# Kernel optimization log

Measured on AMD Instinct MI355X. Metric: run time of the kernel, lower is better.

Reference implementation:

```python
import jax, jax.numpy as jnp
import numpy as np

NUM_GRAPHS = 1024

def setup_inputs() -> dict:
    key = jax.random.key(0)
    ks = jax.random.split(key, 6)
    N, E = 500000, 16000000
    x = jax.random.normal(ks[0], (N, 4), dtype=jnp.float32)
    edge_index = jax.random.randint(ks[1], (2, E), 0, N, dtype=jnp.int32)
    batch = jnp.sort(jax.random.randint(ks[2], (N,), 0, NUM_GRAPHS, dtype=jnp.int32))
    eps = jnp.zeros((), dtype=jnp.float32)
    W1 = jax.random.normal(ks[3], (4, 16), dtype=jnp.float32) * 0.5
    b1 = jnp.zeros((16,), dtype=jnp.float32)
    W2 = jax.random.normal(ks[4], (16, 4), dtype=jnp.float32) * 0.25
    b2 = jnp.zeros((4,), dtype=jnp.float32)
    return {"x": x, "edge_index": edge_index, "batch": batch,
            "eps": eps, "W1": W1, "b1": b1, "W2": W2, "b2": b2}

def reference(x, edge_index, batch, eps, W1, b1, W2, b2):
    N = x.shape[0]
    src, dst = edge_index[0], edge_index[1]
    # GINConv aggregation: sum of neighbor (source) features at each target node
    agg = jax.ops.segment_sum(x[src], dst, num_segments=N)  # [N, 4]
    h = (1.0 + eps) * x + agg
    # 2-layer MLP: Lin(4,16) -> ReLU -> Lin(16,4)
    h = jax.nn.relu(h @ W1 + b1) @ W2 + b2
    h = jax.nn.relu(h)
    # global_mean_pool over batch segment ids
    sums = jax.ops.segment_sum(h, batch, num_segments=NUM_GRAPHS)      # [G, 4]
    cnts = jax.ops.segment_sum(jnp.ones((N,), h.dtype), batch, num_segments=NUM_GRAPHS)
    pooled = sums / jnp.maximum(cnts, 1.0)[:, None]
    return jax.nn.log_softmax(pooled, axis=1)
```

## Files before the change

kernel.cpp:

```cpp
#include <hip/hip_runtime.h>

#define NUM_GRAPHS 1024
#define BIN_BITS 10
#define BIN_SIZE (1 << BIN_BITS)
#define EB 8192
#define STH 512
#define EPT 16
#define ATH 1024
#define ACH 8192
#define AEPT (ACH / ATH)

typedef int v4i __attribute__((ext_vector_type(4)));

__device__ inline unsigned bf16_rn(float f) {
    unsigned u = __float_as_uint(f);
    return (u + 0x7FFFu + ((u >> 16) & 1u)) >> 16;
}
__global__ void prep_kernel(const float4* __restrict__ x, uint2* __restrict__ x16,
                            int N, int* __restrict__ cursor,
                            float* __restrict__ gsum, float* __restrict__ gcnt,
                            int cap) {
    int i = blockIdx.x * blockDim.x + threadIdx.x;
    if (i < 512) cursor[i] = i * cap;
    if (i < NUM_GRAPHS * 4) gsum[i] = 0.0f;
    if (i < NUM_GRAPHS) gcnt[i] = 0.0f;
    if (i < N) {
        float4 v = x[i];
        uint2 r;
        r.x = bf16_rn(v.x) | (bf16_rn(v.y) << 16);
        r.y = bf16_rn(v.z) | (bf16_rn(v.w) << 16);
        x16[i] = r;
    }
}

__global__ void __launch_bounds__(STH) bin_scatter(const int* __restrict__ src,
                                                   const int* __restrict__ dst,
                                                   int* __restrict__ packed,
                                                   int* __restrict__ cursor,
                                                   int E, int cap, int nb) {
    __shared__ int shist[512];
    __shared__ int sprefix[513];
    __shared__ int sgbase[512];
    __shared__ int spacked[EB];
    __shared__ unsigned short sbin[EB];
    __shared__ int wsum[8];

    const int t = threadIdx.x;
    const int lane = t & 63;
    const int wave = t >> 6;
    const int b0 = blockIdx.x * EB;
    const int myBase = b0 + t * EPT;

    for (int j = t; j < 512; j += STH) shist[j] = 0;
    __syncthreads();

    int pv[EPT];
    int bl[EPT];
    const bool full = (myBase + EPT <= E);
    if (full) {
#pragma unroll
        for (int v = 0; v < EPT / 4; ++v) {
            int4 d = *(const int4*)(dst + myBase + v * 4);
            int4 s = *(const int4*)(src + myBase + v * 4);
            int bn, lp;
            bn = ((unsigned)d.x) >> BIN_BITS; lp = atomicAdd(&shist[bn], 1);
            pv[v * 4 + 0] = ((d.x & (BIN_SIZE - 1)) << 19) | s.x;
            bl[v * 4 + 0] = (bn << 13) | lp;
            bn = ((unsigned)d.y) >> BIN_BITS; lp = atomicAdd(&shist[bn], 1);
            pv[v * 4 + 1] = ((d.y & (BIN_SIZE - 1)) << 19) | s.y;
            bl[v * 4 + 1] = (bn << 13) | lp;
            bn = ((unsigned)d.z) >> BIN_BITS; lp = atomicAdd(&shist[bn], 1);
            pv[v * 4 + 2] = ((d.z & (BIN_SIZE - 1)) << 19) | s.z;
            bl[v * 4 + 2] = (bn << 13) | lp;
            bn = ((unsigned)d.w) >> BIN_BITS; lp = atomicAdd(&shist[bn], 1);
            pv[v * 4 + 3] = ((d.w & (BIN_SIZE - 1)) << 19) | s.w;
            bl[v * 4 + 3] = (bn << 13) | lp;
        }
    } else {
#pragma unroll
        for (int i = 0; i < EPT; ++i) {
            int e = myBase + i;
            bool ok = e < E;
            int d = ok ? dst[e] : 0;
            int s = ok ? src[e] : 0;
            int bn = ((unsigned)d) >> BIN_BITS;
            int lp = 0;
            if (ok) lp = atomicAdd(&shist[bn], 1);
            pv[i] = ((d & (BIN_SIZE - 1)) << 19) | s;
            bl[i] = ok ? ((bn << 13) | lp) : -1;
        }
    }
    __syncthreads();

    {
        int v = shist[t];
        int inc = v;
#pragma unroll
        for (int off = 1; off < 64; off <<= 1) {
            int u = __shfl_up(inc, off);
            if (lane >= off) inc += u;
        }
        if (lane == 63) wsum[wave] = inc;
        __syncthreads();
        if (t == 0) {
            int acc = 0;
#pragma unroll
            for (int w = 0; w < 8; ++w) { int c = wsum[w]; wsum[w] = acc; acc += c; }
        }
        __syncthreads();
        sprefix[t + 1] = inc + wsum[wave];
        if (t == 0) sprefix[0] = 0;
        if (t < nb && v > 0) sgbase[t] = atomicAdd(&cursor[t], v);
    }
    __syncthreads();

    if (full) {
#pragma unroll
        for (int i = 0; i < EPT; ++i) {
            int bn = ((unsigned)bl[i]) >> 13;
            int lp = bl[i] & 0x1FFF;
            int idx = sprefix[bn] + lp;
            spacked[idx] = pv[i];
            sbin[idx] = (unsigned short)bn;
        }
    } else {
#pragma unroll
        for (int i = 0; i < EPT; ++i) {
            if (bl[i] >= 0) {
                int bn = ((unsigned)bl[i]) >> 13;
                int lp = bl[i] & 0x1FFF;
                int idx = sprefix[bn] + lp;
                spacked[idx] = pv[i];
                sbin[idx] = (unsigned short)bn;
            }
        }
    }
    __syncthreads();

    int cnt = sprefix[nb < 512 ? nb : 512];
    int totE = E - b0; if (totE < 0) totE = 0;
    if (cnt > totE) cnt = totE;
    for (int j = t; j < cnt; j += STH) {
        int bn = sbin[j];
        int pos = sgbase[bn] + (j - sprefix[bn]);
        if (pos < (bn + 1) * cap)
            __builtin_nontemporal_store(spacked[j], &packed[pos]);
    }
}

__global__ void __launch_bounds__(ATH) bin_accum_mlp_pool(
        const float4* __restrict__ x,
        const uint2* __restrict__ x16,
        const int* __restrict__ packed,
        const int* __restrict__ cursor,
        const int* __restrict__ batch,
        const float* __restrict__ eps_p,
        const float* __restrict__ W1, const float* __restrict__ b1,
        const float* __restrict__ W2, const float* __restrict__ b2,
        float* __restrict__ gsum, float* __restrict__ gcnt,
        int N, int cap) {
    __shared__ int srt[ACH];
    __shared__ int hist[BIN_SIZE];
    __shared__ int pfx[BIN_SIZE + 1];
    __shared__ int wsum[16];

    const int bin = blockIdx.x;
    const int t = threadIdx.x;
    const int lane = t & 63;
    const int wave = t >> 6;

    const int start = bin * cap;
    int end = cursor[bin];
    if (end > start + cap) end = start + cap;

    float a0 = 0.f, a1 = 0.f, a2 = 0.f, a3 = 0.f;

#pragma unroll 1
    for (int cs = start; cs < end; cs += ACH) {
        int ce = cs + ACH; if (ce > end) ce = end;

        hist[t] = 0;
        __syncthreads();

        int dlp[AEPT];
        int sv[AEPT];
#pragma unroll
        for (int i = 0; i < AEPT / 4; ++i) {
            int ebase = cs + (i * ATH + t) * 4;
            v4i p4;
            if (ebase + 3 < ce) {
                p4 = __builtin_nontemporal_load((const v4i*)(packed + ebase));
            } else {
                p4.x = (ebase + 0 < ce) ? packed[ebase + 0] : 0;
                p4.y = (ebase + 1 < ce) ? packed[ebase + 1] : 0;
                p4.z = (ebase + 2 < ce) ? packed[ebase + 2] : 0;
                p4.w = (ebase + 3 < ce) ? packed[ebase + 3] : 0;
            }
#pragma unroll
            for (int k = 0; k < 4; ++k) {
                int p = (k == 0) ? p4.x : (k == 1) ? p4.y : (k == 2) ? p4.z : p4.w;
                bool ok = (ebase + k) < ce;
                int dl = ((unsigned)p) >> 19;
                int lp = 0;
                if (ok) lp = atomicAdd(&hist[dl], 1);
                dlp[i * 4 + k] = ok ? ((dl << 13) | lp) : -1;
                sv[i * 4 + k] = p & 0x7FFFF;
            }
        }
        __syncthreads();

        {
            int v = hist[t];
            int inc = v;
#pragma unroll
            for (int off = 1; off < 64; off <<= 1) {
                int u = __shfl_up(inc, off);
                if (lane >= off) inc += u;
            }
            if (lane == 63) wsum[wave] = inc;
            __syncthreads();
            if (t == 0) {
                int acc = 0;
#pragma unroll
                for (int w = 0; w < 16; ++w) { int c = wsum[w]; wsum[w] = acc; acc += c; }
            }
            __syncthreads();
            pfx[t + 1] = inc + wsum[wave];
            if (t == 0) pfx[0] = 0;
        }
        __syncthreads();

#pragma unroll
        for (int i = 0; i < AEPT; ++i) {
            if (dlp[i] >= 0) {
                int dl = ((unsigned)dlp[i]) >> 13;
                int lp = dlp[i] & 0x1FFF;
                srt[pfx[dl] + lp] = sv[i];
            }
        }
        __syncthreads();

        int jb = pfx[t], je = pfx[t + 1];
        for (int j = jb; j < je; ++j) {
            uint2 v = x16[srt[j]];
            a0 += __uint_as_float(v.x << 16);
            a1 += __uint_as_float(v.x & 0xFFFF0000u);
            a2 += __uint_as_float(v.y << 16);
            a3 += __uint_as_float(v.y & 0xFFFF0000u);
        }
        __syncthreads();
    }

    int n = bin * BIN_SIZE + t;
    bool valid = n < N;
    float o0 = 0.f, o1 = 0.f, o2 = 0.f, o3 = 0.f;
    int g = -1;
    if (valid) {
        float eps = eps_p[0];
        float4 xv = x[n];
        float h0 = (1.0f + eps) * xv.x + a0;
        float h1 = (1.0f + eps) * xv.y + a1;
        float h2 = (1.0f + eps) * xv.z + a2;
        float h3 = (1.0f + eps) * xv.w + a3;

        float tmp[16];
#pragma unroll
        for (int j = 0; j < 16; ++j) {
            float v = b1[j] + h0 * W1[j] + h1 * W1[16 + j] + h2 * W1[32 + j] + h3 * W1[48 + j];
            tmp[j] = v > 0.0f ? v : 0.0f;
        }
        float o[4];
#pragma unroll
        for (int j = 0; j < 4; ++j) {
            float v = b2[j];
#pragma unroll
            for (int k = 0; k < 16; ++k) v += tmp[k] * W2[k * 4 + j];
            o[j] = v > 0.0f ? v : 0.0f;
        }
        o0 = o[0]; o1 = o[1]; o2 = o[2]; o3 = o[3];
        g = batch[n];
    }

    int g0 = __shfl(g, 0);
    bool uni = __all(g == g0);
    if (uni && g0 >= 0) {
#pragma unroll
        for (int off = 32; off > 0; off >>= 1) {
            o0 += __shfl_down(o0, off);
            o1 += __shfl_down(o1, off);
            o2 += __shfl_down(o2, off);
            o3 += __shfl_down(o3, off);
        }
        if ((t & 63) == 0) {
            unsafeAtomicAdd(&gsum[(size_t)g0 * 4 + 0], o0);
            unsafeAtomicAdd(&gsum[(size_t)g0 * 4 + 1], o1);
            unsafeAtomicAdd(&gsum[(size_t)g0 * 4 + 2], o2);
            unsafeAtomicAdd(&gsum[(size_t)g0 * 4 + 3], o3);
            unsafeAtomicAdd(&gcnt[g0], 64.0f);
        }
    } else if (valid) {
        unsafeAtomicAdd(&gsum[(size_t)g * 4 + 0], o0);
        unsafeAtomicAdd(&gsum[(size_t)g * 4 + 1], o1);
        unsafeAtomicAdd(&gsum[(size_t)g * 4 + 2], o2);
        unsafeAtomicAdd(&gsum[(size_t)g * 4 + 3], o3);
        unsafeAtomicAdd(&gcnt[g], 1.0f);
    }
}

__global__ void pool_softmax_kernel(const float* __restrict__ gsum,
                                    const float* __restrict__ gcnt,
                                    float* __restrict__ out) {
    int g = blockIdx.x * blockDim.x + threadIdx.x;
    if (g >= NUM_GRAPHS) return;
    float c = fmaxf(gcnt[g], 1.0f);
    float p0 = gsum[g * 4 + 0] / c;
    float p1 = gsum[g * 4 + 1] / c;
    float p2 = gsum[g * 4 + 2] / c;
    float p3 = gsum[g * 4 + 3] / c;
    float m = fmaxf(fmaxf(p0, p1), fmaxf(p2, p3));
    float s = expf(p0 - m) + expf(p1 - m) + expf(p2 - m) + expf(p3 - m);
    float lse = m + logf(s);
    out[g * 4 + 0] = p0 - lse;
    out[g * 4 + 1] = p1 - lse;
    out[g * 4 + 2] = p2 - lse;
    out[g * 4 + 3] = p3 - lse;
}

__global__ void edge_scatter_kernel(const float4* __restrict__ x,
                                    const int* __restrict__ src,
                                    const int* __restrict__ dst,
                                    float* __restrict__ agg,
                                    int E) {
    int t = blockIdx.x * blockDim.x + threadIdx.x;
    int e = t * 4;
    if (e + 3 < E) {
        int4 s = *(const int4*)(src + e);
        int4 d = *(const int4*)(dst + e);
        float4 xv;
        xv = x[s.x];
        unsafeAtomicAdd(&agg[(size_t)d.x * 4 + 0], xv.x);
        unsafeAtomicAdd(&agg[(size_t)d.x * 4 + 1], xv.y);
        unsafeAtomicAdd(&agg[(size_t)d.x * 4 + 2], xv.z);
        unsafeAtomicAdd(&agg[(size_t)d.x * 4 + 3], xv.w);
        xv = x[s.y];
        unsafeAtomicAdd(&agg[(size_t)d.y * 4 + 0], xv.x);
        unsafeAtomicAdd(&agg[(size_t)d.y * 4 + 1], xv.y);
        unsafeAtomicAdd(&agg[(size_t)d.y * 4 + 2], xv.z);
        unsafeAtomicAdd(&agg[(size_t)d.y * 4 + 3], xv.w);
        xv = x[s.z];
        unsafeAtomicAdd(&agg[(size_t)d.z * 4 + 0], xv.x);
        unsafeAtomicAdd(&agg[(size_t)d.z * 4 + 1], xv.y);
        unsafeAtomicAdd(&agg[(size_t)d.z * 4 + 2], xv.z);
        unsafeAtomicAdd(&agg[(size_t)d.z * 4 + 3], xv.w);
        xv = x[s.w];
        unsafeAtomicAdd(&agg[(size_t)d.w * 4 + 0], xv.x);
        unsafeAtomicAdd(&agg[(size_t)d.w * 4 + 1], xv.y);
        unsafeAtomicAdd(&agg[(size_t)d.w * 4 + 2], xv.z);
        unsafeAtomicAdd(&agg[(size_t)d.w * 4 + 3], xv.w);
    } else {
        for (int i = e; i < E; ++i) {
            int sv = src[i], dv = dst[i];
            float4 xv = x[sv];
            unsafeAtomicAdd(&agg[(size_t)dv * 4 + 0], xv.x);
            unsafeAtomicAdd(&agg[(size_t)dv * 4 + 1], xv.y);
            unsafeAtomicAdd(&agg[(size_t)dv * 4 + 2], xv.z);
            unsafeAtomicAdd(&agg[(size_t)dv * 4 + 3], xv.w);
        }
    }
}

__global__ void node_mlp_pool_kernel(const float4* __restrict__ x,
                                     const float4* __restrict__ agg,
                                     const int* __restrict__ batch,
                                     const float* __restrict__ eps_p,
                                     const float* __restrict__ W1,
                                     const float* __restrict__ b1,
                                     const float* __restrict__ W2,
                                     const float* __restrict__ b2,
                                     float* __restrict__ gsum,
                                     float* __restrict__ gcnt,
                                     int N) {
    int i = blockIdx.x * blockDim.x + threadIdx.x;
    bool valid = i < N;
    float o0 = 0.f, o1 = 0.f, o2 = 0.f, o3 = 0.f;
    int g = -1;
    if (valid) {
        float eps = eps_p[0];
        float4 xv = x[i];
        float4 av = agg[i];
        float h0 = (1.0f + eps) * xv.x + av.x;
        float h1 = (1.0f + eps) * xv.y + av.y;
        float h2 = (1.0f + eps) * xv.z + av.z;
        float h3 = (1.0f + eps) * xv.w + av.w;
        float tmp[16];
#pragma unroll
        for (int j = 0; j < 16; ++j) {
            float v = b1[j] + h0 * W1[j] + h1 * W1[16 + j] + h2 * W1[32 + j] + h3 * W1[48 + j];
            tmp[j] = v > 0.0f ? v : 0.0f;
        }
        float o[4];
#pragma unroll
        for (int j = 0; j < 4; ++j) {
            float v = b2[j];
#pragma unroll
            for (int k = 0; k < 16; ++k) v += tmp[k] * W2[k * 4 + j];
            o[j] = v > 0.0f ? v : 0.0f;
        }
        o0 = o[0]; o1 = o[1]; o2 = o[2]; o3 = o[3];
        g = batch[i];
    }
    int g0 = __shfl(g, 0);
    bool uni = __all(g == g0);
    if (uni && g0 >= 0) {
#pragma unroll
        for (int off = 32; off > 0; off >>= 1) {
            o0 += __shfl_down(o0, off);
            o1 += __shfl_down(o1, off);
            o2 += __shfl_down(o2, off);
            o3 += __shfl_down(o3, off);
        }
        if ((threadIdx.x & 63) == 0) {
            unsafeAtomicAdd(&gsum[(size_t)g0 * 4 + 0], o0);
            unsafeAtomicAdd(&gsum[(size_t)g0 * 4 + 1], o1);
            unsafeAtomicAdd(&gsum[(size_t)g0 * 4 + 2], o2);
            unsafeAtomicAdd(&gsum[(size_t)g0 * 4 + 3], o3);
            unsafeAtomicAdd(&gcnt[g0], 64.0f);
        }
    } else if (valid) {
        unsafeAtomicAdd(&gsum[(size_t)g * 4 + 0], o0);
        unsafeAtomicAdd(&gsum[(size_t)g * 4 + 1], o1);
        unsafeAtomicAdd(&gsum[(size_t)g * 4 + 2], o2);
        unsafeAtomicAdd(&gsum[(size_t)g * 4 + 3], o3);
        unsafeAtomicAdd(&gcnt[g], 1.0f);
    }
}

extern "C" void kernel_launch(void* const* d_in, const int* in_sizes, int n_in,
                              void* d_out, int out_size, void* d_ws, size_t ws_size,
                              hipStream_t stream) {
    const float* x     = (const float*)d_in[0];
    const int*   ei    = (const int*)d_in[1];
    const int*   batch = (const int*)d_in[2];
    const float* eps   = (const float*)d_in[3];
    const float* W1    = (const float*)d_in[4];
    const float* b1    = (const float*)d_in[5];
    const float* W2    = (const float*)d_in[6];
    const float* b2    = (const float*)d_in[7];

    const int N = in_sizes[0] / 4;
    const int E = in_sizes[1] / 2;
    const int* src = ei;
    const int* dst = ei + (size_t)E;

    const int nb = (N + BIN_SIZE - 1) >> BIN_BITS;
    const int epb = (E + nb - 1) / nb;
    int cap = epb + epb / 8 + 1024;
    cap = (cap + 3) & ~3;

    size_t x16_elems = ((size_t)2 * N + 3) & ~(size_t)3;
    size_t packed_elems = ((size_t)nb * cap + 3) & ~(size_t)3;
    size_t need = (x16_elems + packed_elems + 512 + NUM_GRAPHS * 5) * sizeof(float);

    if (nb <= 512 && N < (1 << 19) && need <= ws_size) {
        uint2* x16    = (uint2*)d_ws;
        int*   packed = (int*)d_ws + x16_elems;
        int*   cursor = packed + packed_elems;
        float* gsum   = (float*)(cursor + 512);
        float* gcnt   = gsum + (size_t)NUM_GRAPHS * 4;

        prep_kernel<<<(N + 511) / 512, 512, 0, stream>>>(
            (const float4*)x, x16, N, cursor, gsum, gcnt, cap);

        int nblocks_e = (E + EB - 1) / EB;
        bin_scatter<<<nblocks_e, STH, 0, stream>>>(src, dst, packed, cursor, E, cap, nb);

        bin_accum_mlp_pool<<<nb, ATH, 0, stream>>>(
            (const float4*)x, (const uint2*)x16, packed, cursor, batch, eps,
            W1, b1, W2, b2, gsum, gcnt, N, cap);

        pool_softmax_kernel<<<(NUM_GRAPHS + 255) / 256, 256, 0, stream>>>(
            gsum, gcnt, (float*)d_out);
    } else {
        float* agg  = (float*)d_ws;
        float* gsum = agg + (size_t)N * 4;
        float* gcnt = gsum + (size_t)NUM_GRAPHS * 4;
        size_t zero_bytes = ((size_t)N * 4 + NUM_GRAPHS * 5) * sizeof(float);
        (void)hipMemsetAsync(d_ws, 0, zero_bytes, stream);

        int e4 = (E + 3) / 4;
        edge_scatter_kernel<<<(e4 + 255) / 256, 256, 0, stream>>>(
            (const float4*)x, src, dst, agg, E);

        node_mlp_pool_kernel<<<(N + 255) / 256, 256, 0, stream>>>(
            (const float4*)x, (const float4*)agg, batch, eps, W1, b1, W2, b2,
            gsum, gcnt, N);

        pool_softmax_kernel<<<(NUM_GRAPHS + 255) / 256, 256, 0, stream>>>(
            gsum, gcnt, (float*)d_out);
    }
}
```

Measured before the change: 451.6 us.

## Replace per-chunk LDS counting sort with direct shared-memory float atomics

The accumulation kernel used to sort each chunk of packed edges by local destination, using a histogram, a prefix scan, a scatter and several barriers, and then had each thread sum its own node's neighbors in registers. The new code gathers each source feature directly and adds its four components into per-node shared-memory float arrays with atomicAdd. This removes the sort, the scan and most barriers, and it gathers with more parallelism per thread. In exchange it issues four LDS float atomics per edge, which can contend when many edges share a destination, and the summation order becomes nondeterministic.

```diff
diff --git a/kernel.cpp b/kernel.cpp
--- a/kernel.cpp
+++ b/kernel.cpp
@@ -7,8 +7,6 @@
 #define STH 512
 #define EPT 16
 #define ATH 1024
-#define ACH 8192
-#define AEPT (ACH / ATH)
 
 typedef int v4i __attribute__((ext_vector_type(4)));
 
@@ -159,97 +157,52 @@
         const float* __restrict__ W2, const float* __restrict__ b2,
         float* __restrict__ gsum, float* __restrict__ gcnt,
         int N, int cap) {
-    __shared__ int srt[ACH];
-    __shared__ int hist[BIN_SIZE];
-    __shared__ int pfx[BIN_SIZE + 1];
-    __shared__ int wsum[16];
+    __shared__ float agg0[BIN_SIZE];
+    __shared__ float agg1[BIN_SIZE];
+    __shared__ float agg2[BIN_SIZE];
+    __shared__ float agg3[BIN_SIZE];
 
     const int bin = blockIdx.x;
     const int t = threadIdx.x;
-    const int lane = t & 63;
-    const int wave = t >> 6;
+
+    agg0[t] = 0.0f; agg1[t] = 0.0f; agg2[t] = 0.0f; agg3[t] = 0.0f;
+    __syncthreads();
 
     const int start = bin * cap;
     int end = cursor[bin];
     if (end > start + cap) end = start + cap;
 
-    float a0 = 0.f, a1 = 0.f, a2 = 0.f, a3 = 0.f;
-
-#pragma unroll 1
-    for (int cs = start; cs < end; cs += ACH) {
-        int ce = cs + ACH; if (ce > end) ce = end;
-
-        hist[t] = 0;
-        __syncthreads();
-
-        int dlp[AEPT];
-        int sv[AEPT];
-#pragma unroll
-        for (int i = 0; i < AEPT / 4; ++i) {
-            int ebase = cs + (i * ATH + t) * 4;
-            v4i p4;
-            if (ebase + 3 < ce) {
-                p4 = __builtin_nontemporal_load((const v4i*)(packed + ebase));
-            } else {
-                p4.x = (ebase + 0 < ce) ? packed[ebase + 0] : 0;
-                p4.y = (ebase + 1 < ce) ? packed[ebase + 1] : 0;
-                p4.z = (ebase + 2 < ce) ? packed[ebase + 2] : 0;
-                p4.w = (ebase + 3 < ce) ? packed[ebase + 3] : 0;
-            }
+    for (int e = start + t * 4; e < end; e += ATH * 4) {
+        if (e + 3 < end) {
+            v4i p4 = __builtin_nontemporal_load((const v4i*)(packed + e));
 #pragma unroll
             for (int k = 0; k < 4; ++k) {
                 int p = (k == 0) ? p4.x : (k == 1) ? p4.y : (k == 2) ? p4.z : p4.w;
-                bool ok = (ebase + k) < ce;
                 int dl = ((unsigned)p) >> 19;
-                int lp = 0;
-                if (ok) lp = atomicAdd(&hist[dl], 1);
-                dlp[i * 4 + k] = ok ? ((dl << 13) | lp) : -1;
-                sv[i * 4 + k] = p & 0x7FFFF;
+                uint2 v = x16[p & 0x7FFFF];
+                atomicAdd(&agg0[dl], __uint_as_float(v.x << 16));
+                atomicAdd(&agg1[dl], __uint_as_float(v.x & 0xFFFF0000u));
+                atomicAdd(&agg2[dl], __uint_as_float(v.y << 16));
+                atomicAdd(&agg3[dl], __uint_as_float(v.y & 0xFFFF0000u));
             }
-        }
-        __syncthreads();
-
-        {
-            int v = hist[t];
-            int inc = v;
-#pragma unroll
-            for (int off = 1; off < 64; off <<= 1) {
-                int u = __shfl_up(inc, off);
-                if (lane >= off) inc += u;
+        } else {
+#pragma unroll
+            for (int k = 0; k < 4; ++k) {
+                if (e + k < end) {
+                    int p = packed[e + k];
+                    int dl = ((unsigned)p) >> 19;
+                    uint2 v = x16[p & 0x7FFFF];
+                    atomicAdd(&agg0[dl], __uint_as_float(v.x << 16));
+                    atomicAdd(&agg1[dl], __uint_as_float(v.x & 0xFFFF0000u));
+                    atomicAdd(&agg2[dl], __uint_as_float(v.y << 16));
+                    atomicAdd(&agg3[dl], __uint_as_float(v.y & 0xFFFF0000u));
+                }
             }
-            if (lane == 63) wsum[wave] = inc;
-            __syncthreads();
-            if (t == 0) {
-                int acc = 0;
-#pragma unroll
-                for (int w = 0; w < 16; ++w) { int c = wsum[w]; wsum[w] = acc; acc += c; }
-            }
-            __syncthreads();
-            pfx[t + 1] = inc + wsum[wave];
-            if (t == 0) pfx[0] = 0;
-        }
-        __syncthreads();
-
-#pragma unroll
-        for (int i = 0; i < AEPT; ++i) {
-            if (dlp[i] >= 0) {
-                int dl = ((unsigned)dlp[i]) >> 13;
-                int lp = dlp[i] & 0x1FFF;
-                srt[pfx[dl] + lp] = sv[i];
-            }
-        }
-        __syncthreads();
-
-        int jb = pfx[t], je = pfx[t + 1];
-        for (int j = jb; j < je; ++j) {
-            uint2 v = x16[srt[j]];
-            a0 += __uint_as_float(v.x << 16);
-            a1 += __uint_as_float(v.x & 0xFFFF0000u);
-            a2 += __uint_as_float(v.y << 16);
-            a3 += __uint_as_float(v.y & 0xFFFF0000u);
-        }
-        __syncthreads();
-    }
+        }
+    }
+    __syncthreads();
+
+    const float a0 = agg0[t], a1 = agg1[t], a2 = agg2[t], a3 = agg3[t];
 
     int n = bin * BIN_SIZE + t;
     bool valid = n < N;
```

After: 676.7 us. 1.5x slower.
